# Optimization experiments

Measured on AMD Instinct MI355X. Metric: run time of the kernel, lower is better.

Reference implementation:

```python
import jax, jax.numpy as jnp
import numpy as np

N = 100000
E = 1600000
D_IN = 128
F = 128


def _glorot(key, shape, scale=1.0):
    fan_in, fan_out = shape
    std = jnp.sqrt(2.0 / (fan_in + fan_out))
    return jax.random.normal(key, shape, dtype=jnp.float32) * std * scale


def setup_inputs() -> dict:
    key = jax.random.key(0)
    ks = jax.random.split(key, 10)
    h = jax.random.normal(ks[0], (N, D_IN), dtype=jnp.float32)
    # ensure every node appears as a row (src) so degree >= 1 (no inf in deg**-0.5)
    src_extra = jax.random.randint(ks[1], (E - N,), 0, N, dtype=jnp.int32)
    edge_src = jnp.concatenate([jnp.arange(N, dtype=jnp.int32), src_extra])
    edge_dst = jax.random.randint(ks[2], (E,), 0, N, dtype=jnp.int32)
    # faithful to original: fake indices sampled in [0, E) (jnp indexing clamps)
    src_fake = jax.random.randint(ks[3], (E,), 0, E, dtype=jnp.int32)
    dst_fake = jax.random.randint(ks[4], (E,), 0, E, dtype=jnp.int32)
    w_gcn0 = _glorot(ks[5], (D_IN, F))
    w_gcn1 = _glorot(ks[6], (F, F))
    # small scale on rate0 head to keep exp(sum over F dims) finite in fp32
    w_rate0 = _glorot(ks[7], (F, F), scale=0.05)
    w_rate1 = _glorot(ks[8], (F, 1))
    w_alpha = _glorot(ks[9], (F, 1))
    return {"h": h, "w_gcn0": w_gcn0, "w_gcn1": w_gcn1, "w_rate0": w_rate0,
            "w_rate1": w_rate1, "w_alpha": w_alpha, "edge_src": edge_src,
            "edge_dst": edge_dst, "src_fake": src_fake, "dst_fake": dst_fake}


def _gcn(h, W, norm, edge_src, edge_dst):
    h = h * norm                     # [N, d] degree pre-norm
    h = h @ W                        # dense projection
    h = jax.ops.segment_sum(h[edge_dst], edge_src, num_segments=N)  # a @ h
    return h * norm                  # degree post-norm


def reference(h, w_gcn0, w_gcn1, w_rate0, w_rate1, w_alpha,
              edge_src, edge_dst, src_fake, dst_fake):
    ones = jnp.ones((E,), dtype=h.dtype)
    deg = jax.ops.segment_sum(ones, edge_src, num_segments=N)  # row sums of a
    norm = (deg ** -0.5)[:, None]

    h = _gcn(h, w_gcn0, norm, edge_src, edge_dst)
    h = _gcn(h, w_gcn1, norm, edge_src, edge_dst)

    rate0 = h @ w_rate0   # [N, F]
    rate1 = h @ w_rate1   # [N, 1]
    alpha = h @ w_alpha   # [N, 1]

    src, dst = edge_src, edge_dst
    rate0_real = jnp.exp((rate0[src] + rate0[dst]).sum(-1))
    rate1_real = jnp.exp((rate1[src] + rate1[dst]).sum(-1))
    alpha_real = jax.nn.sigmoid((alpha[src] * alpha[dst]).sum(-1) / alpha.shape[-1] ** 0.5)

    # faithful to original (including rate0+rate1 mix and /shape (not sqrt) in alpha_fake)
    rate0_fake = jnp.exp((rate0[src_fake] + rate1[dst_fake]).sum(-1))
    rate1_fake = jnp.exp((rate1[src_fake] + rate1[dst_fake]).sum(-1))
    alpha_fake = jax.nn.sigmoid((alpha[src] * alpha[dst_fake]).sum(-1) / alpha.shape[-1])

    return jnp.stack([rate0_real, rate1_real, alpha_real,
                      rate0_fake, rate1_fake, alpha_fake])  # [6, E]
```

## Files before the change

kernel.cpp:

```cpp
#include <hip/hip_runtime.h>
#include <math.h>

#define NN 100000
#define EE 1600000
#define KB 256
#define RR 391
#define CAP 8192


__global__ __launch_bounds__(1024) void k_pmat(const float* __restrict__ w_gcn0,
                                               const float* __restrict__ w_gcn1,
                                               const float* __restrict__ w_rate0,
                                               const float* __restrict__ w_rate1,
                                               const float* __restrict__ w_alpha,
                                               float* __restrict__ Pt0, float* __restrict__ Pt1,
                                               float* __restrict__ Pt2, int* __restrict__ gcur) {
    __shared__ float V0[128], V1[128], V2[128];
    __shared__ float Q0[128], Q1[128], Q2[128];
    int t = threadIdx.x;
    if (t < KB) gcur[t] = 0;
    int r = t >> 3, seg = t & 7;
    {
        const float* p = w_rate0 + r * 128 + seg * 16;
        float s = 0.f;
        #pragma unroll
        for (int k = 0; k < 16; ++k) s += p[k];
        s += __shfl_down(s, 4, 8); s += __shfl_down(s, 2, 8); s += __shfl_down(s, 1, 8);
        if (seg == 0) V0[r] = s;
    }
    if (t < 128) { V1[t] = w_rate1[t]; V2[t] = w_alpha[t]; }
    __syncthreads();
    {
        const float* p = w_gcn1 + r * 128 + seg * 16;
        float q0 = 0.f, q1 = 0.f, q2 = 0.f;
        #pragma unroll
        for (int k = 0; k < 16; ++k) {
            float w = p[k]; int j = seg * 16 + k;
            q0 += w * V0[j]; q1 += w * V1[j]; q2 += w * V2[j];
        }
        q0 += __shfl_down(q0, 4, 8); q0 += __shfl_down(q0, 2, 8); q0 += __shfl_down(q0, 1, 8);
        q1 += __shfl_down(q1, 4, 8); q1 += __shfl_down(q1, 2, 8); q1 += __shfl_down(q1, 1, 8);
        q2 += __shfl_down(q2, 4, 8); q2 += __shfl_down(q2, 2, 8); q2 += __shfl_down(q2, 1, 8);
        if (seg == 0) { Q0[r] = q0; Q1[r] = q1; Q2[r] = q2; }
    }
    __syncthreads();
    {
        const float* p = w_gcn0 + r * 128 + seg * 16;
        float q0 = 0.f, q1 = 0.f, q2 = 0.f;
        #pragma unroll
        for (int k = 0; k < 16; ++k) {
            float w = p[k]; int j = seg * 16 + k;
            q0 += w * Q0[j]; q1 += w * Q1[j]; q2 += w * Q2[j];
        }
        q0 += __shfl_down(q0, 4, 8); q0 += __shfl_down(q0, 2, 8); q0 += __shfl_down(q0, 1, 8);
        q1 += __shfl_down(q1, 4, 8); q1 += __shfl_down(q1, 2, 8); q1 += __shfl_down(q1, 1, 8);
        q2 += __shfl_down(q2, 4, 8); q2 += __shfl_down(q2, 2, 8); q2 += __shfl_down(q2, 1, 8);
        if (seg == 0) { Pt0[r] = q0; Pt1[r] = q1; Pt2[r] = q2; }
    }
}


__global__ __launch_bounds__(512) void k_part_proj(const int* __restrict__ src, const int* __restrict__ dst,
                                                   int* __restrict__ gcur, unsigned int* __restrict__ pk,
                                                   const float* __restrict__ h,
                                                   const float* __restrict__ Pt0, const float* __restrict__ Pt1,
                                                   const float* __restrict__ Pt2,
                                                   float4* __restrict__ u4) {
    __shared__ int cnt[KB];
    __shared__ int base[KB];
    __shared__ float sP0[128], sP1[128], sP2[128];
    int t = threadIdx.x;
    int role = blockIdx.x & 1;
    int id = blockIdx.x >> 1;

    if (role == 0) {
        if (t < KB) cnt[t] = 0;
        __syncthreads();
        int e0 = id * 4096;
        unsigned int pkv[8];
        int bkt[8];
        #pragma unroll
        for (int i = 0; i < 8; ++i) {
            int e = e0 + i * 512 + t;
            if (e < EE) {
                int s = src[e];
                int d = dst[e];
                int b = s / RR;
                bkt[i] = b;
                pkv[i] = (unsigned int)d | ((unsigned int)(s - b * RR) << 17);
                atomicAdd(&cnt[b], 1);
            } else bkt[i] = -1;
        }
        __syncthreads();
        if (t < KB) base[t] = cnt[t] ? atomicAdd(&gcur[t], cnt[t]) : 0;
        __syncthreads();
        if (t < KB) cnt[t] = 0;
        __syncthreads();
        #pragma unroll
        for (int i = 0; i < 8; ++i) {
            if (bkt[i] >= 0) {
                int rr = atomicAdd(&cnt[bkt[i]], 1);
                int rel = base[bkt[i]] + rr;
                if (rel < CAP) pk[bkt[i] * CAP + rel] = pkv[i];
            }
        }
    } else {
        if (t < 128) { sP0[t] = Pt0[t]; sP1[t] = Pt1[t]; sP2[t] = Pt2[t]; }
        __syncthreads();
        int hw = t >> 5;
        int l32 = t & 31;
        int c4 = l32 * 4;
        float4 c0 = *(const float4*)(sP0 + c4);
        float4 c1 = *(const float4*)(sP1 + c4);
        float4 c2 = *(const float4*)(sP2 + c4);
        int nlo = id * 256;
        for (int i0 = 0; i0 < 256; i0 += 16) {
            int node = nlo + i0 + hw;
            if (node < NN) {
                float4 hv = *(const float4*)(h + (size_t)node * 128 + c4);
                float p0v = hv.x * c0.x + hv.y * c0.y + hv.z * c0.z + hv.w * c0.w;
                float p1v = hv.x * c1.x + hv.y * c1.y + hv.z * c1.z + hv.w * c1.w;
                float p2v = hv.x * c2.x + hv.y * c2.y + hv.z * c2.z + hv.w * c2.w;
                #pragma unroll
                for (int off = 16; off > 0; off >>= 1) {
                    p0v += __shfl_down(p0v, off, 32);
                    p1v += __shfl_down(p1v, off, 32);
                    p2v += __shfl_down(p2v, off, 32);
                }
                if (l32 == 0) {
                    float* up = (float*)&u4[node];
                    *(float2*)up = make_float2(p0v, p1v);
                    up[2] = p2v;
                }
            }
        }
    }
}


__global__ __launch_bounds__(1024) void k_cnt(const unsigned int* __restrict__ pk,
                                              const int* __restrict__ gcur,
                                              float* __restrict__ nrm, float4* __restrict__ u4) {
    __shared__ int c[RR];
    int b = blockIdx.x;
    int t = threadIdx.x;
    int nlo = b * RR;
    int nn = NN - nlo; if (nn > RR) nn = RR;
    if (nn <= 0) return;
    if (t < RR) c[t] = 0;
    __syncthreads();
    const unsigned int* P = pk + b * CAP;
    int m = gcur[b]; if (m > CAP) m = CAP;
    for (int i = t; i < m; i += 1024) atomicAdd(&c[P[i] >> 17], 1);
    __syncthreads();
    if (t < nn) {
        float nv = rsqrtf((float)c[t]);
        nrm[nlo + t] = nv;
        ((float*)&u4[nlo + t])[3] = nv;
    }
}


template<int MODE>
__global__ __launch_bounds__(1024) void k_agg(const unsigned int* __restrict__ pk,
                                              const int* __restrict__ gcur,
                                              const float4* __restrict__ T, const float* __restrict__ nrm,
                                              float4* __restrict__ outv) {
    __shared__ float s0[RR], s1[RR], s2[RR];
    int b = blockIdx.x;
    int t = threadIdx.x;
    int nlo = b * RR;
    int nn = NN - nlo; if (nn > RR) nn = RR;
    if (nn <= 0) return;
    if (t < RR) { s0[t] = 0.f; s1[t] = 0.f; s2[t] = 0.f; }
    __syncthreads();
    const unsigned int* P = pk + b * CAP;
    int m = gcur[b]; if (m > CAP) m = CAP;
    int i = t;
    for (; i + 1024 < m; i += 2048) {
        unsigned int wa = P[i];
        unsigned int wb = P[i + 1024];
        float4 va = T[wa & 0x1FFFFu];
        float4 vb = T[wb & 0x1FFFFu];
        float ax = va.x, ay = va.y, az = va.z;
        float bx = vb.x, by = vb.y, bz = vb.z;
        if (MODE == 1) { ax *= va.w; ay *= va.w; az *= va.w; bx *= vb.w; by *= vb.w; bz *= vb.w; }
        int ra = (int)(wa >> 17), rb = (int)(wb >> 17);
        atomicAdd(&s0[ra], ax); atomicAdd(&s1[ra], ay); atomicAdd(&s2[ra], az);
        atomicAdd(&s0[rb], bx); atomicAdd(&s1[rb], by); atomicAdd(&s2[rb], bz);
    }
    if (i < m) {
        unsigned int wa = P[i];
        float4 va = T[wa & 0x1FFFFu];
        float ax = va.x, ay = va.y, az = va.z;
        if (MODE == 1) { ax *= va.w; ay *= va.w; az *= va.w; }
        int ra = (int)(wa >> 17);
        atomicAdd(&s0[ra], ax); atomicAdd(&s1[ra], ay); atomicAdd(&s2[ra], az);
    }
    __syncthreads();
    for (int j = t; j < nn; j += 1024) {
        float nv = nrm[nlo + j];
        float sc = (MODE == 1) ? nv * nv : nv;
        outv[nlo + j] = make_float4(sc * s0[j], sc * s1[j], sc * s2[j], 0.f);
    }
}


__global__ __launch_bounds__(256) void k_edge(const int* __restrict__ esrc, const int* __restrict__ edst,
                                              const int* __restrict__ sfake, const int* __restrict__ dfake,
                                              const float4* __restrict__ p4, float* __restrict__ out) {
    int t = threadIdx.x;
    int e0 = blockIdx.x * 1024 + t * 4;
    if (e0 >= EE) return;
    int4 s4  = *(const int4*)(esrc + e0);
    int4 d4  = *(const int4*)(edst + e0);
    int4 sf4 = *(const int4*)(sfake + e0);
    int4 df4 = *(const int4*)(dfake + e0);
    int ss[4] = { s4.x, s4.y, s4.z, s4.w };
    int dd[4] = { d4.x, d4.y, d4.z, d4.w };
    int sf[4] = { sf4.x, sf4.y, sf4.z, sf4.w };
    int df[4] = { df4.x, df4.y, df4.z, df4.w };
    float o0[4], o1[4], o2[4], o3[4], o4[4], o5[4];
    #pragma unroll
    for (int j = 0; j < 4; ++j) {
        int sfj = sf[j]; sfj = sfj < 0 ? 0 : (sfj >= NN ? NN - 1 : sfj);
        int dfj = df[j]; dfj = dfj < 0 ? 0 : (dfj >= NN ? NN - 1 : dfj);
        float4 ps = p4[ss[j]], pd = p4[dd[j]], psf = p4[sfj], pdf = p4[dfj];
        o0[j] = expf(ps.x + pd.x);
        o1[j] = expf(ps.y + pd.y);
        o2[j] = 1.f / (1.f + expf(-(ps.z * pd.z)));
        o3[j] = expf(psf.x + 128.f * pdf.y);
        o4[j] = expf(psf.y + pdf.y);
        o5[j] = 1.f / (1.f + expf(-(ps.z * pdf.z)));
    }
    *(float4*)(out + e0)                  = make_float4(o0[0], o0[1], o0[2], o0[3]);
    *(float4*)(out + (size_t)EE + e0)     = make_float4(o1[0], o1[1], o1[2], o1[3]);
    *(float4*)(out + (size_t)2 * EE + e0) = make_float4(o2[0], o2[1], o2[2], o2[3]);
    *(float4*)(out + (size_t)3 * EE + e0) = make_float4(o3[0], o3[1], o3[2], o3[3]);
    *(float4*)(out + (size_t)4 * EE + e0) = make_float4(o4[0], o4[1], o4[2], o4[3]);
    *(float4*)(out + (size_t)5 * EE + e0) = make_float4(o5[0], o5[1], o5[2], o5[3]);
}


extern "C" void kernel_launch(void* const* d_in, const int* in_sizes, int n_in,
                              void* d_out, int out_size, void* d_ws, size_t ws_size,
                              hipStream_t stream) {
    const float* h       = (const float*)d_in[0];
    const float* w_gcn0  = (const float*)d_in[1];
    const float* w_gcn1  = (const float*)d_in[2];
    const float* w_rate0 = (const float*)d_in[3];
    const float* w_rate1 = (const float*)d_in[4];
    const float* w_alpha = (const float*)d_in[5];
    const int* edge_src  = (const int*)d_in[6];
    const int* edge_dst  = (const int*)d_in[7];
    const int* src_fake  = (const int*)d_in[8];
    const int* dst_fake  = (const int*)d_in[9];
    float* out = (float*)d_out;

    char* p = (char*)d_ws;
    auto alloc = [&](size_t bytes) {
        char* r = p;
        p += (bytes + 255) & ~(size_t)255;
        return r;
    };
    unsigned int* pk = (unsigned int*)alloc((size_t)KB * CAP * 4);
    int* gcur   = (int*)alloc(KB * 4);
    float* nrm  = (float*)alloc((size_t)NN * 4);
    float4* u4  = (float4*)alloc((size_t)NN * 16);
    float4* z4  = (float4*)alloc((size_t)NN * 16);
    float4* p4  = (float4*)alloc((size_t)NN * 16);
    float* Pt0  = (float*)alloc(512);
    float* Pt1  = (float*)alloc(512);
    float* Pt2  = (float*)alloc(512);

    k_pmat<<<1, 1024, 0, stream>>>(w_gcn0, w_gcn1, w_rate0, w_rate1, w_alpha, Pt0, Pt1, Pt2, gcur);
    k_part_proj<<<782, 512, 0, stream>>>(edge_src, edge_dst, gcur, pk, h, Pt0, Pt1, Pt2, u4);
    k_cnt<<<KB, 1024, 0, stream>>>(pk, gcur, nrm, u4);
    k_agg<1><<<KB, 1024, 0, stream>>>(pk, gcur, u4, nrm, z4);
    k_agg<2><<<KB, 1024, 0, stream>>>(pk, gcur, z4, nrm, p4);
    k_edge<<<(EE + 1023) / 1024, 256, 0, stream>>>(edge_src, edge_dst, src_fake, dst_fake, p4, out);
}
```

Before: 222.9 us.

## Regroup pipeline stages: fuse pmat with partition, projection with degree count

The stages are regrouped so the single-block weight-product computation runs as an extra block alongside the edge-partition blocks, and the node projection runs in the same launch as the per-bucket degree count. This takes the serial one-block kernel off the critical path and packs independent work together. The partition now reads edges with contiguous int4 loads per thread, which changes the order edges land in each bucket. A tiny init kernel is added to zero the bucket counters, so there is one extra launch.

```diff
diff --git a/kernel.cpp b/kernel.cpp
--- a/kernel.cpp
+++ b/kernel.cpp
@@ -6,95 +6,64 @@
 #define KB 256
 #define RR 391
 #define CAP 8192
-
-
-__global__ __launch_bounds__(1024) void k_pmat(const float* __restrict__ w_gcn0,
-                                               const float* __restrict__ w_gcn1,
-                                               const float* __restrict__ w_rate0,
-                                               const float* __restrict__ w_rate1,
-                                               const float* __restrict__ w_alpha,
-                                               float* __restrict__ Pt0, float* __restrict__ Pt1,
-                                               float* __restrict__ Pt2, int* __restrict__ gcur) {
-    __shared__ float V0[128], V1[128], V2[128];
-    __shared__ float Q0[128], Q1[128], Q2[128];
+#define PARTB 782
+#define PROJB 391
+
+
+__global__ __launch_bounds__(256) void k_init(int* __restrict__ gcur) {
+    gcur[threadIdx.x] = 0;
+}
+
+
+__global__ __launch_bounds__(256) void k_part_pmat(const int* __restrict__ src, const int* __restrict__ dst,
+                                                   int* __restrict__ gcur, unsigned int* __restrict__ pk,
+                                                   const float* __restrict__ w_gcn0,
+                                                   const float* __restrict__ w_gcn1,
+                                                   const float* __restrict__ w_rate0,
+                                                   const float* __restrict__ w_rate1,
+                                                   const float* __restrict__ w_alpha,
+                                                   float* __restrict__ Pt0, float* __restrict__ Pt1,
+                                                   float* __restrict__ Pt2) {
     int t = threadIdx.x;
-    if (t < KB) gcur[t] = 0;
-    int r = t >> 3, seg = t & 7;
-    {
-        const float* p = w_rate0 + r * 128 + seg * 16;
-        float s = 0.f;
-        #pragma unroll
-        for (int k = 0; k < 16; ++k) s += p[k];
-        s += __shfl_down(s, 4, 8); s += __shfl_down(s, 2, 8); s += __shfl_down(s, 1, 8);
-        if (seg == 0) V0[r] = s;
-    }
-    if (t < 128) { V1[t] = w_rate1[t]; V2[t] = w_alpha[t]; }
-    __syncthreads();
-    {
-        const float* p = w_gcn1 + r * 128 + seg * 16;
-        float q0 = 0.f, q1 = 0.f, q2 = 0.f;
-        #pragma unroll
-        for (int k = 0; k < 16; ++k) {
-            float w = p[k]; int j = seg * 16 + k;
-            q0 += w * V0[j]; q1 += w * V1[j]; q2 += w * V2[j];
-        }
-        q0 += __shfl_down(q0, 4, 8); q0 += __shfl_down(q0, 2, 8); q0 += __shfl_down(q0, 1, 8);
-        q1 += __shfl_down(q1, 4, 8); q1 += __shfl_down(q1, 2, 8); q1 += __shfl_down(q1, 1, 8);
-        q2 += __shfl_down(q2, 4, 8); q2 += __shfl_down(q2, 2, 8); q2 += __shfl_down(q2, 1, 8);
-        if (seg == 0) { Q0[r] = q0; Q1[r] = q1; Q2[r] = q2; }
-    }
-    __syncthreads();
-    {
-        const float* p = w_gcn0 + r * 128 + seg * 16;
-        float q0 = 0.f, q1 = 0.f, q2 = 0.f;
-        #pragma unroll
-        for (int k = 0; k < 16; ++k) {
-            float w = p[k]; int j = seg * 16 + k;
-            q0 += w * Q0[j]; q1 += w * Q1[j]; q2 += w * Q2[j];
-        }
-        q0 += __shfl_down(q0, 4, 8); q0 += __shfl_down(q0, 2, 8); q0 += __shfl_down(q0, 1, 8);
-        q1 += __shfl_down(q1, 4, 8); q1 += __shfl_down(q1, 2, 8); q1 += __shfl_down(q1, 1, 8);
-        q2 += __shfl_down(q2, 4, 8); q2 += __shfl_down(q2, 2, 8); q2 += __shfl_down(q2, 1, 8);
-        if (seg == 0) { Pt0[r] = q0; Pt1[r] = q1; Pt2[r] = q2; }
-    }
-}
-
-
-__global__ __launch_bounds__(512) void k_part_proj(const int* __restrict__ src, const int* __restrict__ dst,
-                                                   int* __restrict__ gcur, unsigned int* __restrict__ pk,
-                                                   const float* __restrict__ h,
-                                                   const float* __restrict__ Pt0, const float* __restrict__ Pt1,
-                                                   const float* __restrict__ Pt2,
-                                                   float4* __restrict__ u4) {
-    __shared__ int cnt[KB];
-    __shared__ int base[KB];
-    __shared__ float sP0[128], sP1[128], sP2[128];
-    int t = threadIdx.x;
-    int role = blockIdx.x & 1;
-    int id = blockIdx.x >> 1;
-
-    if (role == 0) {
-        if (t < KB) cnt[t] = 0;
-        __syncthreads();
-        int e0 = id * 4096;
+    if (blockIdx.x < PARTB) {
+        __shared__ int cnt[KB];
+        __shared__ int base[KB];
+        cnt[t] = 0;
+        __syncthreads();
+        int e0 = blockIdx.x * 2048 + t * 8;
         unsigned int pkv[8];
         int bkt[8];
-        #pragma unroll
-        for (int i = 0; i < 8; ++i) {
-            int e = e0 + i * 512 + t;
-            if (e < EE) {
-                int s = src[e];
-                int d = dst[e];
-                int b = s / RR;
+        if (e0 + 8 <= EE) {
+            int4 sa = *(const int4*)(src + e0);
+            int4 sb = *(const int4*)(src + e0 + 4);
+            int4 da = *(const int4*)(dst + e0);
+            int4 db = *(const int4*)(dst + e0 + 4);
+            int ss[8] = { sa.x, sa.y, sa.z, sa.w, sb.x, sb.y, sb.z, sb.w };
+            int dd[8] = { da.x, da.y, da.z, da.w, db.x, db.y, db.z, db.w };
+            #pragma unroll
+            for (int i = 0; i < 8; ++i) {
+                int b = ss[i] / RR;
                 bkt[i] = b;
-                pkv[i] = (unsigned int)d | ((unsigned int)(s - b * RR) << 17);
+                pkv[i] = (unsigned int)dd[i] | ((unsigned int)(ss[i] - b * RR) << 17);
                 atomicAdd(&cnt[b], 1);
-            } else bkt[i] = -1;
-        }
-        __syncthreads();
-        if (t < KB) base[t] = cnt[t] ? atomicAdd(&gcur[t], cnt[t]) : 0;
-        __syncthreads();
-        if (t < KB) cnt[t] = 0;
+            }
+        } else {
+            #pragma unroll
+            for (int i = 0; i < 8; ++i) {
+                int e = e0 + i;
+                if (e < EE) {
+                    int s = src[e], d = dst[e];
+                    int b = s / RR;
+                    bkt[i] = b;
+                    pkv[i] = (unsigned int)d | ((unsigned int)(s - b * RR) << 17);
+                    atomicAdd(&cnt[b], 1);
+                } else bkt[i] = -1;
+            }
+        }
+        __syncthreads();
+        base[t] = cnt[t] ? atomicAdd(&gcur[t], cnt[t]) : 0;
+        __syncthreads();
+        cnt[t] = 0;
         __syncthreads();
         #pragma unroll
         for (int i = 0; i < 8; ++i) {
@@ -105,6 +74,65 @@
             }
         }
     } else {
+        __shared__ float V0[128], V1[128], V2[128];
+        __shared__ float Q0[128], Q1[128], Q2[128];
+        int r = t >> 1, seg = t & 1;
+        {
+            const float4* p = (const float4*)(w_rate0 + r * 128 + seg * 64);
+            float s = 0.f;
+            #pragma unroll
+            for (int k = 0; k < 16; ++k) { float4 v = p[k]; s += v.x + v.y + v.z + v.w; }
+            s += __shfl_down(s, 1, 2);
+            if (seg == 0) V0[r] = s;
+        }
+        if (t < 128) { V1[t] = w_rate1[t]; V2[t] = w_alpha[t]; }
+        __syncthreads();
+        {
+            const float4* p = (const float4*)(w_gcn1 + r * 128 + seg * 64);
+            float q0 = 0.f, q1 = 0.f, q2 = 0.f;
+            #pragma unroll
+            for (int k = 0; k < 16; ++k) {
+                float4 w = p[k];
+                int j = seg * 64 + k * 4;
+                q0 += w.x * V0[j] + w.y * V0[j+1] + w.z * V0[j+2] + w.w * V0[j+3];
+                q1 += w.x * V1[j] + w.y * V1[j+1] + w.z * V1[j+2] + w.w * V1[j+3];
+                q2 += w.x * V2[j] + w.y * V2[j+1] + w.z * V2[j+2] + w.w * V2[j+3];
+            }
+            q0 += __shfl_down(q0, 1, 2);
+            q1 += __shfl_down(q1, 1, 2);
+            q2 += __shfl_down(q2, 1, 2);
+            if (seg == 0) { Q0[r] = q0; Q1[r] = q1; Q2[r] = q2; }
+        }
+        __syncthreads();
+        {
+            const float4* p = (const float4*)(w_gcn0 + r * 128 + seg * 64);
+            float q0 = 0.f, q1 = 0.f, q2 = 0.f;
+            #pragma unroll
+            for (int k = 0; k < 16; ++k) {
+                float4 w = p[k];
+                int j = seg * 64 + k * 4;
+                q0 += w.x * Q0[j] + w.y * Q0[j+1] + w.z * Q0[j+2] + w.w * Q0[j+3];
+                q1 += w.x * Q1[j] + w.y * Q1[j+1] + w.z * Q1[j+2] + w.w * Q1[j+3];
+                q2 += w.x * Q2[j] + w.y * Q2[j+1] + w.z * Q2[j+2] + w.w * Q2[j+3];
+            }
+            q0 += __shfl_down(q0, 1, 2);
+            q1 += __shfl_down(q1, 1, 2);
+            q2 += __shfl_down(q2, 1, 2);
+            if (seg == 0) { Pt0[r] = q0; Pt1[r] = q1; Pt2[r] = q2; }
+        }
+    }
+}
+
+
+__global__ __launch_bounds__(512) void k_proj_cnt(const unsigned int* __restrict__ pk,
+                                                  const int* __restrict__ gcur,
+                                                  const float* __restrict__ h,
+                                                  const float* __restrict__ Pt0, const float* __restrict__ Pt1,
+                                                  const float* __restrict__ Pt2,
+                                                  float* __restrict__ nrm, float4* __restrict__ u4) {
+    int t = threadIdx.x;
+    if (blockIdx.x < PROJB) {
+        __shared__ float sP0[128], sP1[128], sP2[128];
         if (t < 128) { sP0[t] = Pt0[t]; sP1[t] = Pt1[t]; sP2[t] = Pt2[t]; }
         __syncthreads();
         int hw = t >> 5;
@@ -113,7 +141,7 @@
         float4 c0 = *(const float4*)(sP0 + c4);
         float4 c1 = *(const float4*)(sP1 + c4);
         float4 c2 = *(const float4*)(sP2 + c4);
-        int nlo = id * 256;
+        int nlo = blockIdx.x * 256;
         for (int i0 = 0; i0 < 256; i0 += 16) {
             int node = nlo + i0 + hw;
             if (node < NN) {
@@ -134,29 +162,23 @@
                 }
             }
         }
-    }
-}
-
-
-__global__ __launch_bounds__(1024) void k_cnt(const unsigned int* __restrict__ pk,
-                                              const int* __restrict__ gcur,
-                                              float* __restrict__ nrm, float4* __restrict__ u4) {
-    __shared__ int c[RR];
-    int b = blockIdx.x;
-    int t = threadIdx.x;
-    int nlo = b * RR;
-    int nn = NN - nlo; if (nn > RR) nn = RR;
-    if (nn <= 0) return;
-    if (t < RR) c[t] = 0;
-    __syncthreads();
-    const unsigned int* P = pk + b * CAP;
-    int m = gcur[b]; if (m > CAP) m = CAP;
-    for (int i = t; i < m; i += 1024) atomicAdd(&c[P[i] >> 17], 1);
-    __syncthreads();
-    if (t < nn) {
-        float nv = rsqrtf((float)c[t]);
-        nrm[nlo + t] = nv;
-        ((float*)&u4[nlo + t])[3] = nv;
+    } else {
+        __shared__ int c[RR];
+        int b = blockIdx.x - PROJB;
+        int nlo = b * RR;
+        int nn = NN - nlo; if (nn > RR) nn = RR;
+        if (nn <= 0) return;
+        if (t < RR) c[t] = 0;
+        __syncthreads();
+        const unsigned int* P = pk + b * CAP;
+        int m = gcur[b]; if (m > CAP) m = CAP;
+        for (int i = t; i < m; i += 512) atomicAdd(&c[P[i] >> 17], 1);
+        __syncthreads();
+        if (t < nn) {
+            float nv = rsqrtf((float)c[t]);
+            nrm[nlo + t] = nv;
+            ((float*)&u4[nlo + t])[3] = nv;
+        }
     }
 }
 
@@ -273,9 +295,11 @@
     float* Pt1  = (float*)alloc(512);
     float* Pt2  = (float*)alloc(512);
 
-    k_pmat<<<1, 1024, 0, stream>>>(w_gcn0, w_gcn1, w_rate0, w_rate1, w_alpha, Pt0, Pt1, Pt2, gcur);
-    k_part_proj<<<782, 512, 0, stream>>>(edge_src, edge_dst, gcur, pk, h, Pt0, Pt1, Pt2, u4);
-    k_cnt<<<KB, 1024, 0, stream>>>(pk, gcur, nrm, u4);
+    k_init<<<1, KB, 0, stream>>>(gcur);
+    k_part_pmat<<<PARTB + 1, 256, 0, stream>>>(edge_src, edge_dst, gcur, pk,
+                                               w_gcn0, w_gcn1, w_rate0, w_rate1, w_alpha,
+                                               Pt0, Pt1, Pt2);
+    k_proj_cnt<<<PROJB + KB, 512, 0, stream>>>(pk, gcur, h, Pt0, Pt1, Pt2, nrm, u4);
     k_agg<1><<<KB, 1024, 0, stream>>>(pk, gcur, u4, nrm, z4);
     k_agg<2><<<KB, 1024, 0, stream>>>(pk, gcur, z4, nrm, p4);
     k_edge<<<(EE + 1023) / 1024, 256, 0, stream>>>(edge_src, edge_dst, src_fake, dst_fake, p4, out);
```

After: 239.0 us. 1.07x slower.

## Fuse count and aggregation kernels using in-kernel grid barriers

Applied to the files above, without the earlier changes.

Merges the degree-count kernel into the partition/projection kernel: projection blocks spin-wait on a global counter until all partition blocks finish, then compute norms. The two aggregation passes are fused into one kernel with a grid-wide atomic barrier between them. Partition loads are also vectorised to int4 with contiguous per-thread edges. This removes two kernel launches and their tail gaps, but the spin-wait barriers assume all participating blocks are co-resident and can deadlock or serialize if they are not.

```diff
diff --git a/kernel.cpp b/kernel.cpp
--- a/kernel.cpp
+++ b/kernel.cpp
@@ -6,6 +6,7 @@
 #define KB 256
 #define RR 391
 #define CAP 8192
+#define NPART 391
 
 
 __global__ __launch_bounds__(1024) void k_pmat(const float* __restrict__ w_gcn0,
@@ -14,11 +15,13 @@
                                                const float* __restrict__ w_rate1,
                                                const float* __restrict__ w_alpha,
                                                float* __restrict__ Pt0, float* __restrict__ Pt1,
-                                               float* __restrict__ Pt2, int* __restrict__ gcur) {
+                                               float* __restrict__ Pt2, int* __restrict__ gcur,
+                                               int* __restrict__ flags) {
     __shared__ float V0[128], V1[128], V2[128];
     __shared__ float Q0[128], Q1[128], Q2[128];
     int t = threadIdx.x;
     if (t < KB) gcur[t] = 0;
+    if (t == 1023) { flags[0] = 0; flags[1] = 0; }
     int r = t >> 3, seg = t & 7;
     {
         const float* p = w_rate0 + r * 128 + seg * 16;
@@ -60,15 +63,17 @@
 }
 
 
-__global__ __launch_bounds__(512) void k_part_proj(const int* __restrict__ src, const int* __restrict__ dst,
-                                                   int* __restrict__ gcur, unsigned int* __restrict__ pk,
-                                                   const float* __restrict__ h,
-                                                   const float* __restrict__ Pt0, const float* __restrict__ Pt1,
-                                                   const float* __restrict__ Pt2,
-                                                   float4* __restrict__ u4) {
+__global__ __launch_bounds__(512) void k_d1(const int* __restrict__ src, const int* __restrict__ dst,
+                                            int* __restrict__ gcur, unsigned int* __restrict__ pk,
+                                            const float* __restrict__ h,
+                                            const float* __restrict__ Pt0, const float* __restrict__ Pt1,
+                                            const float* __restrict__ Pt2,
+                                            float* __restrict__ nrm, float4* __restrict__ u4,
+                                            int* __restrict__ partdone) {
     __shared__ int cnt[KB];
     __shared__ int base[KB];
     __shared__ float sP0[128], sP1[128], sP2[128];
+    __shared__ int c[RR];
     int t = threadIdx.x;
     int role = blockIdx.x & 1;
     int id = blockIdx.x >> 1;
@@ -76,20 +81,35 @@
     if (role == 0) {
         if (t < KB) cnt[t] = 0;
         __syncthreads();
-        int e0 = id * 4096;
+        int e0 = id * 4096 + t * 8;
         unsigned int pkv[8];
         int bkt[8];
-        #pragma unroll
-        for (int i = 0; i < 8; ++i) {
-            int e = e0 + i * 512 + t;
-            if (e < EE) {
-                int s = src[e];
-                int d = dst[e];
-                int b = s / RR;
+        if (e0 + 8 <= EE) {
+            int4 sa = *(const int4*)(src + e0);
+            int4 sb = *(const int4*)(src + e0 + 4);
+            int4 da = *(const int4*)(dst + e0);
+            int4 db = *(const int4*)(dst + e0 + 4);
+            int ss[8] = { sa.x, sa.y, sa.z, sa.w, sb.x, sb.y, sb.z, sb.w };
+            int dd[8] = { da.x, da.y, da.z, da.w, db.x, db.y, db.z, db.w };
+            #pragma unroll
+            for (int i = 0; i < 8; ++i) {
+                int b = ss[i] / RR;
                 bkt[i] = b;
-                pkv[i] = (unsigned int)d | ((unsigned int)(s - b * RR) << 17);
+                pkv[i] = (unsigned int)dd[i] | ((unsigned int)(ss[i] - b * RR) << 17);
                 atomicAdd(&cnt[b], 1);
-            } else bkt[i] = -1;
+            }
+        } else {
+            #pragma unroll
+            for (int i = 0; i < 8; ++i) {
+                int e = e0 + i;
+                if (e < EE) {
+                    int s = src[e], d = dst[e];
+                    int b = s / RR;
+                    bkt[i] = b;
+                    pkv[i] = (unsigned int)d | ((unsigned int)(s - b * RR) << 17);
+                    atomicAdd(&cnt[b], 1);
+                } else bkt[i] = -1;
+            }
         }
         __syncthreads();
         if (t < KB) base[t] = cnt[t] ? atomicAdd(&gcur[t], cnt[t]) : 0;
@@ -104,6 +124,9 @@
                 if (rel < CAP) pk[bkt[i] * CAP + rel] = pkv[i];
             }
         }
+        __threadfence();
+        __syncthreads();
+        if (t == 0) atomicAdd(partdone, 1);
     } else {
         if (t < 128) { sP0[t] = Pt0[t]; sP1[t] = Pt1[t]; sP2[t] = Pt2[t]; }
         __syncthreads();
@@ -134,44 +157,39 @@
                 }
             }
         }
-    }
-}
-
-
-__global__ __launch_bounds__(1024) void k_cnt(const unsigned int* __restrict__ pk,
-                                              const int* __restrict__ gcur,
-                                              float* __restrict__ nrm, float4* __restrict__ u4) {
-    __shared__ int c[RR];
-    int b = blockIdx.x;
-    int t = threadIdx.x;
-    int nlo = b * RR;
-    int nn = NN - nlo; if (nn > RR) nn = RR;
-    if (nn <= 0) return;
-    if (t < RR) c[t] = 0;
-    __syncthreads();
-    const unsigned int* P = pk + b * CAP;
-    int m = gcur[b]; if (m > CAP) m = CAP;
-    for (int i = t; i < m; i += 1024) atomicAdd(&c[P[i] >> 17], 1);
-    __syncthreads();
-    if (t < nn) {
-        float nv = rsqrtf((float)c[t]);
-        nrm[nlo + t] = nv;
-        ((float*)&u4[nlo + t])[3] = nv;
-    }
-}
-
-
-template<int MODE>
-__global__ __launch_bounds__(1024) void k_agg(const unsigned int* __restrict__ pk,
-                                              const int* __restrict__ gcur,
-                                              const float4* __restrict__ T, const float* __restrict__ nrm,
-                                              float4* __restrict__ outv) {
+        if (id < KB) {
+            if (t < RR) c[t] = 0;
+            if (t == 0) {
+                while (atomicAdd(partdone, 0) < NPART) __builtin_amdgcn_s_sleep(2);
+            }
+            __syncthreads();
+            __threadfence();
+            const unsigned int* P = pk + id * CAP;
+            int m = gcur[id]; if (m > CAP) m = CAP;
+            for (int i = t; i < m; i += 512) atomicAdd(&c[P[i] >> 17], 1);
+            __syncthreads();
+            int nlo2 = id * RR;
+            int nn = NN - nlo2; if (nn > RR) nn = RR;
+            if (t < nn) {
+                float nv = rsqrtf((float)c[t]);
+                nrm[nlo2 + t] = nv;
+                ((float*)&u4[nlo2 + t])[3] = nv;
+            }
+        }
+    }
+}
+
+
+__global__ __launch_bounds__(1024) void k_agg12(const unsigned int* __restrict__ pk,
+                                                const int* __restrict__ gcur,
+                                                const float4* __restrict__ u4, const float* __restrict__ nrm,
+                                                float4* __restrict__ z4, float4* __restrict__ p4,
+                                                int* __restrict__ aggdone) {
     __shared__ float s0[RR], s1[RR], s2[RR];
     int b = blockIdx.x;
     int t = threadIdx.x;
     int nlo = b * RR;
     int nn = NN - nlo; if (nn > RR) nn = RR;
-    if (nn <= 0) return;
     if (t < RR) { s0[t] = 0.f; s1[t] = 0.f; s2[t] = 0.f; }
     __syncthreads();
     const unsigned int* P = pk + b * CAP;
@@ -180,28 +198,54 @@
     for (; i + 1024 < m; i += 2048) {
         unsigned int wa = P[i];
         unsigned int wb = P[i + 1024];
-        float4 va = T[wa & 0x1FFFFu];
-        float4 vb = T[wb & 0x1FFFFu];
-        float ax = va.x, ay = va.y, az = va.z;
-        float bx = vb.x, by = vb.y, bz = vb.z;
-        if (MODE == 1) { ax *= va.w; ay *= va.w; az *= va.w; bx *= vb.w; by *= vb.w; bz *= vb.w; }
+        float4 va = u4[wa & 0x1FFFFu];
+        float4 vb = u4[wb & 0x1FFFFu];
         int ra = (int)(wa >> 17), rb = (int)(wb >> 17);
-        atomicAdd(&s0[ra], ax); atomicAdd(&s1[ra], ay); atomicAdd(&s2[ra], az);
-        atomicAdd(&s0[rb], bx); atomicAdd(&s1[rb], by); atomicAdd(&s2[rb], bz);
+        atomicAdd(&s0[ra], va.x * va.w); atomicAdd(&s1[ra], va.y * va.w); atomicAdd(&s2[ra], va.z * va.w);
+        atomicAdd(&s0[rb], vb.x * vb.w); atomicAdd(&s1[rb], vb.y * vb.w); atomicAdd(&s2[rb], vb.z * vb.w);
     }
     if (i < m) {
         unsigned int wa = P[i];
-        float4 va = T[wa & 0x1FFFFu];
-        float ax = va.x, ay = va.y, az = va.z;
-        if (MODE == 1) { ax *= va.w; ay *= va.w; az *= va.w; }
+        float4 va = u4[wa & 0x1FFFFu];
         int ra = (int)(wa >> 17);
-        atomicAdd(&s0[ra], ax); atomicAdd(&s1[ra], ay); atomicAdd(&s2[ra], az);
+        atomicAdd(&s0[ra], va.x * va.w); atomicAdd(&s1[ra], va.y * va.w); atomicAdd(&s2[ra], va.z * va.w);
     }
     __syncthreads();
     for (int j = t; j < nn; j += 1024) {
         float nv = nrm[nlo + j];
-        float sc = (MODE == 1) ? nv * nv : nv;
-        outv[nlo + j] = make_float4(sc * s0[j], sc * s1[j], sc * s2[j], 0.f);
+        float sc = nv * nv;
+        z4[nlo + j] = make_float4(sc * s0[j], sc * s1[j], sc * s2[j], 0.f);
+    }
+    __threadfence();
+    __syncthreads();
+    if (t == 0) {
+        atomicAdd(aggdone, 1);
+        while (atomicAdd(aggdone, 0) < KB) __builtin_amdgcn_s_sleep(2);
+    }
+    __syncthreads();
+    __threadfence();
+    if (t < RR) { s0[t] = 0.f; s1[t] = 0.f; s2[t] = 0.f; }
+    __syncthreads();
+    i = t;
+    for (; i + 1024 < m; i += 2048) {
+        unsigned int wa = P[i];
+        unsigned int wb = P[i + 1024];
+        float4 va = z4[wa & 0x1FFFFu];
+        float4 vb = z4[wb & 0x1FFFFu];
+        int ra = (int)(wa >> 17), rb = (int)(wb >> 17);
+        atomicAdd(&s0[ra], va.x); atomicAdd(&s1[ra], va.y); atomicAdd(&s2[ra], va.z);
+        atomicAdd(&s0[rb], vb.x); atomicAdd(&s1[rb], vb.y); atomicAdd(&s2[rb], vb.z);
+    }
+    if (i < m) {
+        unsigned int wa = P[i];
+        float4 va = z4[wa & 0x1FFFFu];
+        int ra = (int)(wa >> 17);
+        atomicAdd(&s0[ra], va.x); atomicAdd(&s1[ra], va.y); atomicAdd(&s2[ra], va.z);
+    }
+    __syncthreads();
+    for (int j = t; j < nn; j += 1024) {
+        float nv = nrm[nlo + j];
+        p4[nlo + j] = make_float4(nv * s0[j], nv * s1[j], nv * s2[j], 0.f);
     }
 }
 
@@ -265,6 +309,7 @@
     };
     unsigned int* pk = (unsigned int*)alloc((size_t)KB * CAP * 4);
     int* gcur   = (int*)alloc(KB * 4);
+    int* flags  = (int*)alloc(256);
     float* nrm  = (float*)alloc((size_t)NN * 4);
     float4* u4  = (float4*)alloc((size_t)NN * 16);
     float4* z4  = (float4*)alloc((size_t)NN * 16);
@@ -273,10 +318,10 @@
     float* Pt1  = (float*)alloc(512);
     float* Pt2  = (float*)alloc(512);
 
-    k_pmat<<<1, 1024, 0, stream>>>(w_gcn0, w_gcn1, w_rate0, w_rate1, w_alpha, Pt0, Pt1, Pt2, gcur);
-    k_part_proj<<<782, 512, 0, stream>>>(edge_src, edge_dst, gcur, pk, h, Pt0, Pt1, Pt2, u4);
-    k_cnt<<<KB, 1024, 0, stream>>>(pk, gcur, nrm, u4);
-    k_agg<1><<<KB, 1024, 0, stream>>>(pk, gcur, u4, nrm, z4);
-    k_agg<2><<<KB, 1024, 0, stream>>>(pk, gcur, z4, nrm, p4);
+    k_pmat<<<1, 1024, 0, stream>>>(w_gcn0, w_gcn1, w_rate0, w_rate1, w_alpha,
+                                   Pt0, Pt1, Pt2, gcur, flags);
+    k_d1<<<782, 512, 0, stream>>>(edge_src, edge_dst, gcur, pk, h, Pt0, Pt1, Pt2,
+                                  nrm, u4, &flags[0]);
+    k_agg12<<<KB, 1024, 0, stream>>>(pk, gcur, u4, nrm, z4, p4, &flags[1]);
     k_edge<<<(EE + 1023) / 1024, 256, 0, stream>>>(edge_src, edge_dst, src_fake, dst_fake, p4, out);
 }
```

Result: slower. 659.5 us (+195.9%).
